# Optimization experiments

Measured on AMD Instinct MI355X. Metric: run time of the kernel, lower is better.

## Reference

```python
import jax, jax.numpy as jnp
import numpy as np

B, T, N, F_, H, C, E = 8, 16, 1024, 128, 8, 32, 32768
D = H * C  # 256 = hidden_channels * num_heads
NEG_SLOPE = 0.2


def setup_inputs() -> dict:
    key = jax.random.key(0)
    ks = jax.random.split(key, 16)
    p = lambda k, shape: (jax.random.normal(k, shape, jnp.float32) * 0.05)
    inp = {
        "x": jax.random.normal(ks[0], (B, T, N, F_), jnp.float32),
        "edge_index": jax.random.randint(ks[1], (2, E), 0, N, jnp.int64),
        "edge_weight": jax.random.uniform(ks[2], (E,), jnp.float32),
        # GAT layer 1
        "W1": p(ks[3], (F_, D)), "att_src1": p(ks[4], (H, C)),
        "att_dst1": p(ks[5], (H, C)), "b1": jnp.zeros((D,), jnp.float32),
        # GAT layer 2
        "W2": p(ks[6], (D, D)), "att_src2": p(ks[7], (H, C)),
        "att_dst2": p(ks[8], (H, C)), "b2": jnp.zeros((D,), jnp.float32),
        # LSTM (torch gate order: i, f, g, o)
        "lstm_Wih": p(ks[9], (4 * D, D)), "lstm_Whh": p(ks[10], (4 * D, D)),
        "lstm_bih": jnp.zeros((4 * D,), jnp.float32),
        "lstm_bhh": jnp.zeros((4 * D,), jnp.float32),
        # edge predictors
        "Wp": p(ks[11], (1, D)), "bp": jnp.zeros((1,), jnp.float32),
        "Wc": p(ks[12], (1, D)), "bc": jnp.zeros((1,), jnp.float32),
    }
    return inp


def _gat_layer(x2d, src, dst, W, a_src, a_dst, b):
    # x2d: [N, Fin]; src/dst: [Et] (self-loops already appended)
    h = (x2d @ W).reshape(N, H, C)              # [N, H, C]
    es = jnp.sum(h * a_src, axis=-1)            # [N, H]
    ed = jnp.sum(h * a_dst, axis=-1)            # [N, H]
    e = jax.nn.leaky_relu(es[src] + ed[dst], NEG_SLOPE)  # [Et, H]
    m = jax.ops.segment_max(e, dst, num_segments=N)      # [N, H]
    m = jnp.where(jnp.isfinite(m), m, 0.0)
    pnum = jnp.exp(e - m[dst])                  # [Et, H]
    denom = jax.ops.segment_sum(pnum, dst, num_segments=N)
    alpha = pnum / (denom[dst] + 1e-16)         # segment softmax over incoming edges
    out = jax.ops.segment_sum(alpha[:, :, None] * h[src], dst, num_segments=N)
    return out.reshape(N, D) + b                # concat heads + bias


def _forward(x, edge_index, edge_weight, W1, att_src1, att_dst1, b1,
             W2, att_src2, att_dst2, b2, lstm_Wih, lstm_Whh, lstm_bih,
             lstm_bhh, Wp, bp, Wc, bc):
    # GATConv ignores edge_weight when edge_dim is None (lin_edge is None).
    sl = jnp.arange(N, dtype=edge_index.dtype)
    src = jnp.concatenate([edge_index[0], sl])  # add_self_loops=True
    dst = jnp.concatenate([edge_index[1], sl])

    def per_graph(xi):  # xi: [N, F_]
        hh = jax.nn.relu(_gat_layer(xi, src, dst, W1, att_src1, att_dst1, b1))
        hh = jax.nn.relu(_gat_layer(hh, src, dst, W2, att_src2, att_dst2, b2))
        return hh  # [N, D]

    # stack timesteps then batches == reshape to [B*T, N, F_]
    hall = jax.vmap(per_graph)(x.reshape(B * T, N, F_))  # [B*T, N, D]

    # LSTM over the node dimension (batch_first=True, batch=B*T, seq=N)
    def step(carry, xt):
        hprev, cprev = carry
        z = xt @ lstm_Wih.T + hprev @ lstm_Whh.T + lstm_bih + lstm_bhh
        i, f, g, o = jnp.split(z, 4, axis=-1)
        c = jax.nn.sigmoid(f) * cprev + jax.nn.sigmoid(i) * jnp.tanh(g)
        hcur = jax.nn.sigmoid(o) * jnp.tanh(c)
        return (hcur, hcur * 0 + c)[0:1] * 0 or ((hcur, c), hcur)

    def step2(carry, xt):
        hprev, cprev = carry
        z = xt @ lstm_Wih.T + hprev @ lstm_Whh.T + lstm_bih + lstm_bhh
        i, f, g, o = jnp.split(z, 4, axis=-1)
        c = jax.nn.sigmoid(f) * cprev + jax.nn.sigmoid(i) * jnp.tanh(g)
        hcur = jax.nn.sigmoid(o) * jnp.tanh(c)
        return (hcur, c), hcur

    init = (jnp.zeros((B * T, D), hall.dtype), jnp.zeros((B * T, D), hall.dtype))
    _, hs = jax.lax.scan(step2, init, jnp.swapaxes(hall, 0, 1))  # [N, B*T, D]
    out = jnp.swapaxes(hs, 0, 1)      # [B*T, N, D]

    xsel = out[::T]                   # [B, N, D]
    xflat = xsel.reshape(B * N, D)
    xe = xflat[edge_index[0]] * xflat[edge_index[1]]  # [E, D]
    edge_weights_pred = xe @ Wp.T + bp                # [E, 1]
    logits = (xe @ Wc.T + bc).squeeze(-1)             # [E]
    return edge_weights_pred, logits


def reference(x, edge_index, edge_weight, W1, att_src1, att_dst1, b1,
              W2, att_src2, att_dst2, b2, lstm_Wih, lstm_Whh, lstm_bih,
              lstm_bhh, Wp, bp, Wc, bc):
    return _forward(x, edge_index, edge_weight, W1, att_src1, att_dst1, b1,
                    W2, att_src2, att_dst2, b2, lstm_Wih, lstm_Whh, lstm_bih,
                    lstm_bhh, Wp, bp, Wc, bc)
```

## Files before the change

### kernel.cpp

```cpp
#include <hip/hip_runtime.h>
#include <math.h>

#define NN 1024
#define FF 128
#define DD 256
#define HH 8
#define CC 32
#define EE 32768
#define NEDGE (EE + NN)

__device__ __forceinline__ float sigf(float x) { return 1.0f / (1.0f + expf(-x)); }
__device__ __forceinline__ float fsig(float x) { return 1.0f / (1.0f + __expf(-x)); }
__device__ __forceinline__ float ftanh(float x) { return 2.0f / (1.0f + __expf(-2.0f * x)) - 1.0f; }

__device__ __forceinline__ void barrier_lds() {
  asm volatile("s_waitcnt lgkmcnt(0)" ::: "memory");
  __builtin_amdgcn_sched_barrier(0);
  __builtin_amdgcn_s_barrier();
}

__global__ void k_count(const int* __restrict__ ei, int* __restrict__ count) {
  int k = blockIdx.x * blockDim.x + threadIdx.x;
  if (k >= NEDGE) return;
  int d = (k < EE) ? ei[EE + k] : (k - EE);
  atomicAdd(&count[d], 1);
}

__global__ void k_scan(const int* __restrict__ count, int* __restrict__ rowptr, int* __restrict__ cursor) {
  __shared__ int buf[NN];
  int t = threadIdx.x;
  int c = count[t];
  buf[t] = c;
  __syncthreads();
  for (int off = 1; off < NN; off <<= 1) {
    int add = (t >= off) ? buf[t - off] : 0;
    __syncthreads();
    buf[t] += add;
    __syncthreads();
  }
  int inc = buf[t];
  rowptr[t] = inc - c;
  cursor[t] = inc - c;
  if (t == NN - 1) rowptr[NN] = inc;
}

__global__ void k_scatter(const int* __restrict__ ei, int* __restrict__ cursor, int* __restrict__ csrc) {
  int k = blockIdx.x * blockDim.x + threadIdx.x;
  if (k >= NEDGE) return;
  int s, d;
  if (k < EE) { s = ei[k]; d = ei[EE + k]; }
  else        { s = k - EE; d = k - EE; }
  int pos = atomicAdd(&cursor[d], 1);
  csrc[pos] = s;
}

template<bool BT, bool ADDB>
__global__ __launch_bounds__(256) void k_gemm(const float* __restrict__ A, const float* __restrict__ B,
    const float* __restrict__ bias1, const float* __restrict__ bias2, float* __restrict__ C,
    int M, int N, int K) {
  __shared__ float At[64][17];
  __shared__ float Bt[16][65];
  const int tid = threadIdx.x;
  const int m0 = blockIdx.x * 64, n0 = blockIdx.y * 64;
  const int tx = tid & 15, ty = tid >> 4;
  float acc[4][4] = {{0.f, 0.f, 0.f, 0.f}};
  for (int k0 = 0; k0 < K; k0 += 16) {
    {
      int rr = tid >> 2, kl = (tid & 3) * 4;
      float4 a = *(const float4*)(A + (m0 + rr) * K + k0 + kl);
      At[rr][kl] = a.x; At[rr][kl + 1] = a.y; At[rr][kl + 2] = a.z; At[rr][kl + 3] = a.w;
    }
    if (BT) {
      int nn = tid >> 2, kl = (tid & 3) * 4;
      float4 b = *(const float4*)(B + (n0 + nn) * K + k0 + kl);
      Bt[kl][nn] = b.x; Bt[kl + 1][nn] = b.y; Bt[kl + 2][nn] = b.z; Bt[kl + 3][nn] = b.w;
    } else {
      int kk = tid >> 4, nn = (tid & 15) * 4;
      float4 b = *(const float4*)(B + (k0 + kk) * N + n0 + nn);
      Bt[kk][nn] = b.x; Bt[kk][nn + 1] = b.y; Bt[kk][nn + 2] = b.z; Bt[kk][nn + 3] = b.w;
    }
    __syncthreads();
    #pragma unroll
    for (int kk = 0; kk < 16; ++kk) {
      float av[4], bv[4];
      #pragma unroll
      for (int i = 0; i < 4; ++i) av[i] = At[ty * 4 + i][kk];
      #pragma unroll
      for (int jj = 0; jj < 4; ++jj) bv[jj] = Bt[kk][tx * 4 + jj];
      #pragma unroll
      for (int i = 0; i < 4; ++i)
        #pragma unroll
        for (int jj = 0; jj < 4; ++jj)
          acc[i][jj] = fmaf(av[i], bv[jj], acc[i][jj]);
    }
    __syncthreads();
  }
  #pragma unroll
  for (int i = 0; i < 4; ++i) {
    #pragma unroll
    for (int jj = 0; jj < 4; ++jj) {
      int n = n0 + tx * 4 + jj;
      float v = acc[i][jj];
      if (ADDB) v += bias1[n] + bias2[n];
      C[(m0 + ty * 4 + i) * N + n] = v;
    }
  }
}

__global__ __launch_bounds__(256) void k_att(const float* __restrict__ h, const float* __restrict__ asrc,
    const float* __restrict__ adst, float* __restrict__ es, float* __restrict__ ed) {
  int n = blockIdx.x;
  int hd = threadIdx.x >> 5, c = threadIdx.x & 31;
  float hv = h[n * DD + hd * CC + c];
  float e1 = hv * asrc[hd * CC + c];
  float e2 = hv * adst[hd * CC + c];
  #pragma unroll
  for (int msk = 1; msk < 32; msk <<= 1) { e1 += __shfl_xor(e1, msk); e2 += __shfl_xor(e2, msk); }
  if (c == 0) { es[n * HH + hd] = e1; ed[n * HH + hd] = e2; }
}

__global__ __launch_bounds__(256) void k_agg(const float* __restrict__ h, const float* __restrict__ es,
    const float* __restrict__ ed, const float* __restrict__ bias, const int* __restrict__ rowptr,
    const int* __restrict__ csrc, float* __restrict__ out) {
  int w = blockIdx.x * 4 + (threadIdx.x >> 6);
  int lane = threadIdx.x & 63;
  int n = w >> 3, hd = w & 7;
  int lo = rowptr[n], hi = rowptr[n + 1];
  float edn = ed[n * HH + hd];
  float m = -1e30f;
  for (int k = lo + lane; k < hi; k += 64) {
    int s = csrc[k];
    float e = es[s * HH + hd] + edn;
    e = (e > 0.f) ? e : 0.2f * e;
    m = fmaxf(m, e);
  }
  #pragma unroll
  for (int msk = 1; msk < 64; msk <<= 1) m = fmaxf(m, __shfl_xor(m, msk));
  float den = 0.f;
  for (int k = lo + lane; k < hi; k += 64) {
    int s = csrc[k];
    float e = es[s * HH + hd] + edn;
    e = (e > 0.f) ? e : 0.2f * e;
    den += expf(e - m);
  }
  #pragma unroll
  for (int msk = 1; msk < 64; msk <<= 1) den += __shfl_xor(den, msk);
  float inv = 1.0f / (den + 1e-16f);
  int c = lane & 31, halfsel = lane >> 5;
  float acc = 0.f;
  for (int k = lo + halfsel; k < hi; k += 2) {
    int s = csrc[k];
    float e = es[s * HH + hd] + edn;
    e = (e > 0.f) ? e : 0.2f * e;
    float al = expf(e - m) * inv;
    acc += al * h[s * DD + hd * CC + c];
  }
  acc += __shfl_down(acc, 32);
  if (lane < 32) {
    float v = acc + bias[hd * CC + c];
    out[n * DD + hd * CC + c] = fmaxf(v, 0.f);
  }
}

__global__ __launch_bounds__(512, 1) void k_lstm(const float* __restrict__ xW,
    const float* __restrict__ Whh, unsigned long long* __restrict__ sw,
    float* __restrict__ hs) {
  const int j = blockIdx.x;
  const int t = threadIdx.x;
  const int r = t >> 2, qt = t & 3;
  const int g = r >> 5, kl = r & 31;
  const int grow = g * 256 + j * 32 + kl;
  __shared__ float hlds[DD];
  __shared__ float zlds[128];

  float wa[64];
  {
    const float4* W4 = (const float4*)(Whh + grow * DD + qt * 64);
    #pragma unroll
    for (int q = 0; q < 16; ++q) {
      const int qp = (q + 4 * qt) & 15;
      float4 tmp = W4[qp];
      asm volatile("v_accvgpr_write_b32 %0, %1" : "=a"(wa[4 * q + 0]) : "v"(tmp.x));
      asm volatile("v_accvgpr_write_b32 %0, %1" : "=a"(wa[4 * q + 1]) : "v"(tmp.y));
      asm volatile("v_accvgpr_write_b32 %0, %1" : "=a"(wa[4 * q + 2]) : "v"(tmp.z));
      asm volatile("v_accvgpr_write_b32 %0, %1" : "=a"(wa[4 * q + 3]) : "v"(tmp.w));
    }
  }
  if (t < DD) hlds[t] = 0.f;
  float creg = 0.f;
  float xwv = (qt == 0) ? xW[grow] : 0.f;
  int bud = 1 << 22;
  __syncthreads();

  for (int s = 0; s < NN; ++s) {
    const float4* h4 = (const float4*)hlds + qt * 16;
    float ac4[4] = {0.f, 0.f, 0.f, 0.f};
    #pragma unroll
    for (int q = 0; q < 16; ++q) {
      const int qp = (q + 4 * qt) & 15;
      float4 hv = h4[qp];
      float w0, w1, w2, w3;
      asm volatile("v_accvgpr_read_b32 %0, %1" : "=v"(w0) : "a"(wa[4 * q + 0]));
      asm volatile("v_accvgpr_read_b32 %0, %1" : "=v"(w1) : "a"(wa[4 * q + 1]));
      asm volatile("v_accvgpr_read_b32 %0, %1" : "=v"(w2) : "a"(wa[4 * q + 2]));
      asm volatile("v_accvgpr_read_b32 %0, %1" : "=v"(w3) : "a"(wa[4 * q + 3]));
      ac4[q & 3] = fmaf(w0, hv.x, ac4[q & 3]);
      ac4[q & 3] = fmaf(w1, hv.y, ac4[q & 3]);
      ac4[q & 3] = fmaf(w2, hv.z, ac4[q & 3]);
      ac4[q & 3] = fmaf(w3, hv.w, ac4[q & 3]);
    }
    float acc = (ac4[0] + ac4[1]) + (ac4[2] + ac4[3]);
    acc += __shfl_xor(acc, 1);
    acc += __shfl_xor(acc, 2);
    if (qt == 0) zlds[r] = acc + xwv;
    barrier_lds();

    const int par = (s + 1) & 1;
    const unsigned int tag = (unsigned int)(s + 1);
    float xw_next = (qt == 0 && s + 1 < NN) ? xW[(s + 1) * 1024 + grow] : 0.f;

    if (t < 32) {
      float iv = zlds[t], fv = zlds[32 + t], gv = zlds[64 + t], ov = zlds[96 + t];
      creg = fsig(fv) * creg + fsig(iv) * ftanh(gv);
      float hn = fsig(ov) * ftanh(creg);
      int col = j * 32 + t;
      hlds[col] = hn;
      unsigned long long pk = ((unsigned long long)__float_as_uint(hn) << 32) | tag;
      __hip_atomic_store(&sw[par * DD + col], pk, __ATOMIC_RELAXED, __HIP_MEMORY_SCOPE_AGENT);
      hs[s * DD + col] = hn;
    } else if (t >= 64 && t < 288) {
      int pi = t - 64;
      int peer = j + 1 + (pi >> 5); if (peer >= 8) peer -= 8;
      int col = peer * 32 + (pi & 31);
      int idx = par * DD + col;
      unsigned long long a;
      for (;;) {
        a = __hip_atomic_load(&sw[idx], __ATOMIC_RELAXED, __HIP_MEMORY_SCOPE_AGENT);
        if ((unsigned int)(a & 0xffffffffULL) == tag) break;
        if (--bud <= 0) break;
      }
      hlds[col] = __uint_as_float((unsigned int)(a >> 32));
    }
    barrier_lds();
    xwv = xw_next;
  }
}

__global__ __launch_bounds__(256) void k_edges(const float* __restrict__ hs, const int* __restrict__ ei,
    const float* __restrict__ Wp, const float* __restrict__ bp,
    const float* __restrict__ Wc, const float* __restrict__ bc, float* __restrict__ out) {
  int widx = threadIdx.x >> 6, lane = threadIdx.x & 63;
  int k = blockIdx.x * 4 + widx;
  int sIdx = ei[k], dIdx = ei[EE + k];
  float4 u = ((const float4*)(hs + sIdx * DD))[lane];
  float4 v = ((const float4*)(hs + dIdx * DD))[lane];
  float4 wp = ((const float4*)Wp)[lane];
  float4 wc = ((const float4*)Wc)[lane];
  float x0 = u.x * v.x, x1 = u.y * v.y, x2 = u.z * v.z, x3 = u.w * v.w;
  float ap = x0 * wp.x + x1 * wp.y + x2 * wp.z + x3 * wp.w;
  float ac = x0 * wc.x + x1 * wc.y + x2 * wc.z + x3 * wc.w;
  #pragma unroll
  for (int msk = 1; msk < 64; msk <<= 1) { ap += __shfl_xor(ap, msk); ac += __shfl_xor(ac, msk); }
  if (lane == 0) { out[k] = ap + bp[0]; out[EE + k] = ac + bc[0]; }
}

extern "C" void kernel_launch(void* const* d_in, const int* in_sizes, int n_in,
                              void* d_out, int out_size, void* d_ws, size_t ws_size,
                              hipStream_t stream) {
  const float* x       = (const float*)d_in[0];
  const int* ei        = (const int*)d_in[1];
  const float* W1      = (const float*)d_in[3];
  const float* as1     = (const float*)d_in[4];
  const float* ad1     = (const float*)d_in[5];
  const float* b1      = (const float*)d_in[6];
  const float* W2      = (const float*)d_in[7];
  const float* as2     = (const float*)d_in[8];
  const float* ad2     = (const float*)d_in[9];
  const float* b2      = (const float*)d_in[10];
  const float* Wih     = (const float*)d_in[11];
  const float* Whh     = (const float*)d_in[12];
  const float* bih     = (const float*)d_in[13];
  const float* bhh     = (const float*)d_in[14];
  const float* Wp      = (const float*)d_in[15];
  const float* bp      = (const float*)d_in[16];
  const float* Wc      = (const float*)d_in[17];
  const float* bc      = (const float*)d_in[18];
  float* out = (float*)d_out;

  char* ws = (char*)d_ws;
  int* counts                = (int*)(ws + 0);
  unsigned long long* sloww  = (unsigned long long*)(ws + 4096);
  int* rowptr                = (int*)(ws + 8192);
  int* cursor                = (int*)(ws + 16384);
  int* csrc                  = (int*)(ws + 20480);
  float* es                  = (float*)(ws + 163840);
  float* ed                  = (float*)(ws + 196608);
  float* buf0                = (float*)(ws + 229376);
  float* buf1                = (float*)(ws + 1277952);
  float* xW                  = (float*)(ws + 2326528);
  float* hsall               = (float*)(ws + 6520832);

  hipMemsetAsync(ws, 0, 8192, stream);

  k_count  <<<(NEDGE + 255) / 256, 256, 0, stream>>>(ei, counts);
  k_scan   <<<1, 1024, 0, stream>>>(counts, rowptr, cursor);
  k_scatter<<<(NEDGE + 255) / 256, 256, 0, stream>>>(ei, cursor, csrc);

  k_gemm<false, false><<<dim3(16, 4), 256, 0, stream>>>(x, W1, nullptr, nullptr, buf0, NN, DD, FF);
  k_att<<<NN, 256, 0, stream>>>(buf0, as1, ad1, es, ed);
  k_agg<<<NN * HH / 4, 256, 0, stream>>>(buf0, es, ed, b1, rowptr, csrc, buf1);

  k_gemm<false, false><<<dim3(16, 4), 256, 0, stream>>>(buf1, W2, nullptr, nullptr, buf0, NN, DD, DD);
  k_att<<<NN, 256, 0, stream>>>(buf0, as2, ad2, es, ed);
  k_agg<<<NN * HH / 4, 256, 0, stream>>>(buf0, es, ed, b2, rowptr, csrc, buf1);

  k_gemm<true, true><<<dim3(16, 16), 256, 0, stream>>>(buf1, Wih, bih, bhh, xW, NN, 1024, DD);

  k_lstm<<<8, 512, 0, stream>>>(xW, Whh, sloww, hsall);

  k_edges<<<EE / 4, 256, 0, stream>>>(hsall, ei, Wp, bp, Wc, bc, out);
}
```

Baseline: 1.978 ms.

## Use per-block mailboxes for LSTM hidden-state exchange and keep Whh in VGPRs

The sequential LSTM kernel now pushes each new hidden slice into a private mailbox per consumer block instead of one shared slot that all peers poll. Two waves split the seven remote stores, and each consumer spins only on its own local copy, which cuts contention on shared cache lines during the cross-block handshake every step. The recurrent weights also move from AGPRs, read back with explicit accvgpr instructions, into ordinary vector registers. The costs are more global stores per step, a larger workspace memset, and higher VGPR pressure.

```diff
diff --git a/kernel.cpp b/kernel.cpp
--- a/kernel.cpp
+++ b/kernel.cpp
@@ -9,7 +9,8 @@
 #define EE 32768
 #define NEDGE (EE + NN)
 
-__device__ __forceinline__ float sigf(float x) { return 1.0f / (1.0f + expf(-x)); }
+typedef float f32x4 __attribute__((ext_vector_type(4)));
+
 __device__ __forceinline__ float fsig(float x) { return 1.0f / (1.0f + __expf(-x)); }
 __device__ __forceinline__ float ftanh(float x) { return 2.0f / (1.0f + __expf(-2.0f * x)) - 1.0f; }
 
@@ -163,7 +164,7 @@
 }
 
 __global__ __launch_bounds__(512, 1) void k_lstm(const float* __restrict__ xW,
-    const float* __restrict__ Whh, unsigned long long* __restrict__ sw,
+    const float* __restrict__ Whh, unsigned long long* __restrict__ mbox,
     float* __restrict__ hs) {
   const int j = blockIdx.x;
   const int t = threadIdx.x;
@@ -173,18 +174,13 @@
   __shared__ float hlds[DD];
   __shared__ float zlds[128];
 
-  float wa[64];
+  f32x4 w[16];
   {
-    const float4* W4 = (const float4*)(Whh + grow * DD + qt * 64);
-    #pragma unroll
-    for (int q = 0; q < 16; ++q) {
-      const int qp = (q + 4 * qt) & 15;
-      float4 tmp = W4[qp];
-      asm volatile("v_accvgpr_write_b32 %0, %1" : "=a"(wa[4 * q + 0]) : "v"(tmp.x));
-      asm volatile("v_accvgpr_write_b32 %0, %1" : "=a"(wa[4 * q + 1]) : "v"(tmp.y));
-      asm volatile("v_accvgpr_write_b32 %0, %1" : "=a"(wa[4 * q + 2]) : "v"(tmp.z));
-      asm volatile("v_accvgpr_write_b32 %0, %1" : "=a"(wa[4 * q + 3]) : "v"(tmp.w));
-    }
+    const f32x4* W4 = (const f32x4*)(Whh + grow * DD + qt * 64);
+    #pragma unroll
+    for (int q = 0; q < 16; ++q) w[q] = W4[(q + 4 * qt) & 15];
+    #pragma unroll
+    for (int q = 0; q < 16; ++q) asm volatile("" : "+v"(w[q]));
   }
   if (t < DD) hlds[t] = 0.f;
   float creg = 0.f;
@@ -193,21 +189,16 @@
   __syncthreads();
 
   for (int s = 0; s < NN; ++s) {
-    const float4* h4 = (const float4*)hlds + qt * 16;
+    const f32x4* h4 = (const f32x4*)hlds + qt * 16;
     float ac4[4] = {0.f, 0.f, 0.f, 0.f};
     #pragma unroll
     for (int q = 0; q < 16; ++q) {
-      const int qp = (q + 4 * qt) & 15;
-      float4 hv = h4[qp];
-      float w0, w1, w2, w3;
-      asm volatile("v_accvgpr_read_b32 %0, %1" : "=v"(w0) : "a"(wa[4 * q + 0]));
-      asm volatile("v_accvgpr_read_b32 %0, %1" : "=v"(w1) : "a"(wa[4 * q + 1]));
-      asm volatile("v_accvgpr_read_b32 %0, %1" : "=v"(w2) : "a"(wa[4 * q + 2]));
-      asm volatile("v_accvgpr_read_b32 %0, %1" : "=v"(w3) : "a"(wa[4 * q + 3]));
-      ac4[q & 3] = fmaf(w0, hv.x, ac4[q & 3]);
-      ac4[q & 3] = fmaf(w1, hv.y, ac4[q & 3]);
-      ac4[q & 3] = fmaf(w2, hv.z, ac4[q & 3]);
-      ac4[q & 3] = fmaf(w3, hv.w, ac4[q & 3]);
+      f32x4 hv = h4[(q + 4 * qt) & 15];
+      f32x4 wv = w[q];
+      ac4[q & 3] = fmaf(wv.x, hv.x, ac4[q & 3]);
+      ac4[q & 3] = fmaf(wv.y, hv.y, ac4[q & 3]);
+      ac4[q & 3] = fmaf(wv.z, hv.z, ac4[q & 3]);
+      ac4[q & 3] = fmaf(wv.w, hv.w, ac4[q & 3]);
     }
     float acc = (ac4[0] + ac4[1]) + (ac4[2] + ac4[3]);
     acc += __shfl_xor(acc, 1);
@@ -219,23 +210,38 @@
     const unsigned int tag = (unsigned int)(s + 1);
     float xw_next = (qt == 0 && s + 1 < NN) ? xW[(s + 1) * 1024 + grow] : 0.f;
 
-    if (t < 32) {
-      float iv = zlds[t], fv = zlds[32 + t], gv = zlds[64 + t], ov = zlds[96 + t];
+    if (t < 64) {
+      int lane = t & 31;
+      float iv = zlds[lane], fv = zlds[32 + lane], gv = zlds[64 + lane], ov = zlds[96 + lane];
       creg = fsig(fv) * creg + fsig(iv) * ftanh(gv);
       float hn = fsig(ov) * ftanh(creg);
-      int col = j * 32 + t;
-      hlds[col] = hn;
+      int col = j * 32 + lane;
       unsigned long long pk = ((unsigned long long)__float_as_uint(hn) << 32) | tag;
-      __hip_atomic_store(&sw[par * DD + col], pk, __ATOMIC_RELAXED, __HIP_MEMORY_SCOPE_AGENT);
-      hs[s * DD + col] = hn;
-    } else if (t >= 64 && t < 288) {
+      if (t < 32) {
+        #pragma unroll
+        for (int po = 1; po <= 3; ++po) {
+          int p = j + po; if (p >= 8) p -= 8;
+          __hip_atomic_store(&mbox[(p * 2 + par) * DD + col], pk,
+                             __ATOMIC_RELAXED, __HIP_MEMORY_SCOPE_AGENT);
+        }
+        hlds[col] = hn;
+        hs[s * DD + col] = hn;
+      } else {
+        #pragma unroll
+        for (int po = 4; po <= 7; ++po) {
+          int p = j + po; if (p >= 8) p -= 8;
+          __hip_atomic_store(&mbox[(p * 2 + par) * DD + col], pk,
+                             __ATOMIC_RELAXED, __HIP_MEMORY_SCOPE_AGENT);
+        }
+      }
+    } else if (t < 288) {
       int pi = t - 64;
       int peer = j + 1 + (pi >> 5); if (peer >= 8) peer -= 8;
       int col = peer * 32 + (pi & 31);
-      int idx = par * DD + col;
+      unsigned long long* wp = &mbox[(j * 2 + par) * DD + col];
       unsigned long long a;
       for (;;) {
-        a = __hip_atomic_load(&sw[idx], __ATOMIC_RELAXED, __HIP_MEMORY_SCOPE_AGENT);
+        a = __hip_atomic_load(wp, __ATOMIC_RELAXED, __HIP_MEMORY_SCOPE_AGENT);
         if ((unsigned int)(a & 0xffffffffULL) == tag) break;
         if (--bud <= 0) break;
       }
@@ -289,18 +295,18 @@
 
   char* ws = (char*)d_ws;
   int* counts                = (int*)(ws + 0);
-  unsigned long long* sloww  = (unsigned long long*)(ws + 4096);
-  int* rowptr                = (int*)(ws + 8192);
-  int* cursor                = (int*)(ws + 16384);
-  int* csrc                  = (int*)(ws + 20480);
-  float* es                  = (float*)(ws + 163840);
-  float* ed                  = (float*)(ws + 196608);
-  float* buf0                = (float*)(ws + 229376);
-  float* buf1                = (float*)(ws + 1277952);
-  float* xW                  = (float*)(ws + 2326528);
-  float* hsall               = (float*)(ws + 6520832);
-
-  hipMemsetAsync(ws, 0, 8192, stream);
+  unsigned long long* mbox   = (unsigned long long*)(ws + 4096);
+  int* rowptr                = (int*)(ws + 36864);
+  int* cursor                = (int*)(ws + 45056);
+  int* csrc                  = (int*)(ws + 49152);
+  float* es                  = (float*)(ws + 188416);
+  float* ed                  = (float*)(ws + 221184);
+  float* buf0                = (float*)(ws + 253952);
+  float* buf1                = (float*)(ws + 1302528);
+  float* xW                  = (float*)(ws + 2351104);
+  float* hsall               = (float*)(ws + 6545408);
+
+  hipMemsetAsync(ws, 0, 36864, stream);
 
   k_count  <<<(NEDGE + 255) / 256, 256, 0, stream>>>(ei, counts);
   k_scan   <<<1, 1024, 0, stream>>>(counts, rowptr, cursor);
@@ -316,7 +322,7 @@
 
   k_gemm<true, true><<<dim3(16, 16), 256, 0, stream>>>(buf1, Wih, bih, bhh, xW, NN, 1024, DD);
 
-  k_lstm<<<8, 512, 0, stream>>>(xW, Whh, sloww, hsall);
+  k_lstm<<<8, 512, 0, stream>>>(xW, Whh, mbox, hsall);
 
   k_edges<<<EE / 4, 256, 0, stream>>>(hsall, ei, Wp, bp, Wc, bc, out);
 }
```

Measured after the change: 1.875 ms (median of 2 runs). -5.2%, faster.
